# Kernel optimization log

Measured on AMD Instinct MI355X. Metric: run time of the kernel, lower is better.

## Reference

```python
import jax, jax.numpy as jnp
import numpy as np

TOKENS, IN_F, OUT_F = 8192, 4096, 4096

def setup_inputs() -> dict:
    key = jax.random.key(0)
    k1, k2, k3, k4 = jax.random.split(key, 4)
    # int8 activations and weights in [-127, 127]
    x = jax.random.randint(k1, (TOKENS, IN_F), -127, 128, dtype=jnp.int32).astype(jnp.int8)
    weight = jax.random.randint(k2, (OUT_F, IN_F), -127, 128, dtype=jnp.int32).astype(jnp.int8)  # [out, in]
    # static per-output-channel dequant scale (fp16), small so fp16 output doesn't overflow
    dequant_scale = (jax.random.uniform(k3, (OUT_F,), dtype=jnp.float32) * 1e-3).astype(jnp.float16)
    bias = (jax.random.normal(k4, (OUT_F,), dtype=jnp.float32)).astype(jnp.float16)
    return {"x": x, "weight": weight, "dequant_scale": dequant_scale, "bias": bias}

def reference(x, weight, dequant_scale, bias):
    # int8 GEMM with int32 accumulation: [tokens, in] @ [in, out] -> [tokens, out]
    acc = jax.lax.dot_general(
        x, weight.T,
        dimension_numbers=(((1,), (0,)), ((), ())),
        preferred_element_type=jnp.int32,
    )
    # static per-output-channel dequant, cast to fp16, add fp16 bias
    out = (acc.astype(jnp.float32) * dequant_scale.astype(jnp.float32)[None, :]).astype(jnp.float16)
    out = out + bias[None, :]
    # module returns (output, output_bias)
    return (out, bias)
```

## Files before the change

### kernel.cpp

```cpp
#include <hip/hip_runtime.h>
#include <hip/hip_fp16.h>
#include <stdint.h>

typedef __attribute__((ext_vector_type(4))) int int32x4;

#define TOKENS 8192
#define IN_F   4096
#define OUT_F  4096
#define BM 256
#define BN 256
#define BK 128
#define NT (IN_F / BK)

__global__ __launch_bounds__(256)
void pack_kernel(const int* __restrict__ src, uint32_t* __restrict__ dst, int n4)
{
    for (int i = blockIdx.x * 256 + threadIdx.x; i < n4; i += gridDim.x * 256) {
        int32x4 v = ((const int32x4*)src)[i];
        dst[i] = (uint32_t)(v[0] & 0xff) | ((uint32_t)(v[1] & 0xff) << 8) |
                 ((uint32_t)(v[2] & 0xff) << 16) | ((uint32_t)v[3] << 24);
    }
}

__global__ __launch_bounds__(512, 2)
void w8a8_gemm_kernel(const int8_t* __restrict__ x,
                      const int8_t* __restrict__ w,
                      const float* __restrict__ scale,
                      const float* __restrict__ bias,
                      float* __restrict__ out)
{
    __shared__ int8_t lA[2 * 256 * 128];
    __shared__ int8_t lB[2 * 256 * 128];

    const int tid = threadIdx.x;
    const int wv  = tid >> 6;
    const int l   = tid & 63;
    const int wrow = (wv >> 2) * 128;
    const int wcol = (wv & 3) * 64;

    const int bn = blockIdx.x;
    const int bm = blockIdx.y;

    const int8_t* baseA = x + (size_t)bm * BM * IN_F;
    const int8_t* baseB = w + (size_t)bn * BN * IN_F;

    const int seg0 = wv * 2, seg1 = wv * 2 + 1;
    const int r8   = l >> 3;
    const int swc  = (((l & 7) ^ r8) << 4);

    const int fr  = l & 15;
    const int xk  = (l & 7) << 4;
    const int cb0 = (l >> 4) << 4;

    int32x4 acc[8][4];
#pragma unroll
    for (int m = 0; m < 8; ++m)
#pragma unroll
        for (int n = 0; n < 4; ++n)
            acc[m][n] = (int32x4){0, 0, 0, 0};

    int32x4 aF[4][2];
    int32x4 bF[2][2];

    auto stage_half = [&](int h4) {
        const int kt_ = h4 >> 2;
        const int wh_ = h4 & 3;
        const int8_t* sb = (wh_ < 2) ? baseA : baseB;
        int8_t* db = ((wh_ < 2) ? lA : lB) + ((kt_ & 1) << 15) + ((wh_ & 1) << 14);
        const size_t co = (size_t)kt_ * BK + swc;
        const size_t rb = (size_t)((wh_ & 1) * 128 + r8);
        __builtin_amdgcn_global_load_lds(
            (const __attribute__((address_space(1))) void*)(sb + (rb + seg0 * 8) * IN_F + co),
            (__attribute__((address_space(3))) void*)(db + seg0 * 1024), 16, 0, 0);
        __builtin_amdgcn_global_load_lds(
            (const __attribute__((address_space(1))) void*)(sb + (rb + seg1 * 8) * IN_F + co),
            (__attribute__((address_space(3))) void*)(db + seg1 * 1024), 16, 0, 0);
    };
    auto stage_tile = [&](int tt) {
        stage_half(4 * tt + 0); stage_half(4 * tt + 1);
        stage_half(4 * tt + 2); stage_half(4 * tt + 3);
    };

#define LOADA(MH)                                                                     \
    do {                                                                              \
        _Pragma("unroll") for (int j = 0; j < 4; ++j)                                 \
        _Pragma("unroll") for (int ks = 0; ks < 2; ++ks)                              \
            aF[j][ks] = *(const int32x4*)&lAb[(wrow + ((MH)*4 + j) * 16 + fr) * 128 + \
                                              (((ks * 64) + cb0) ^ xk)];              \
    } while (0)

#define LOADB(NH)                                                                     \
    do {                                                                              \
        _Pragma("unroll") for (int j2 = 0; j2 < 2; ++j2)                              \
        _Pragma("unroll") for (int ks = 0; ks < 2; ++ks)                              \
            bF[j2][ks] = *(const int32x4*)&lBb[(wcol + ((NH)*2 + j2) * 16 + fr) * 128 + \
                                               (((ks * 64) + cb0) ^ xk)];             \
    } while (0)

#define MMAQ(MH, NH)                                                                  \
    do {                                                                              \
        _Pragma("unroll") for (int j = 0; j < 4; ++j)                                 \
        _Pragma("unroll") for (int j2 = 0; j2 < 2; ++j2)                              \
        _Pragma("unroll") for (int ks = 0; ks < 2; ++ks)                              \
            acc[(MH)*4 + j][(NH)*2 + j2] = __builtin_amdgcn_mfma_i32_16x16x64_i8(     \
                aF[j][ks], bF[j2][ks], acc[(MH)*4 + j][(NH)*2 + j2], 0, 0, 0);        \
    } while (0)

#define PH(MH, NH)                                                                    \
    do {                                                                              \
        __builtin_amdgcn_s_barrier();                                                 \
        __builtin_amdgcn_s_setprio(1);                                                \
        MMAQ(MH, NH);                                                                 \
        __builtin_amdgcn_s_setprio(0);                                                \
        __builtin_amdgcn_s_barrier();                                                 \
    } while (0)

    stage_tile(0);
    asm volatile("s_waitcnt vmcnt(0)" ::: "memory");
    __builtin_amdgcn_s_barrier();

    for (int t = 0; t < NT; ++t) {
        const int8_t* lAb = lA + ((t & 1) << 15);
        const int8_t* lBb = lB + ((t & 1) << 15);
        const bool pre = (t + 1 < NT);
        if (pre) stage_tile(t + 1);

        LOADA(0); LOADB(0); PH(0, 0);
        LOADB(1);           PH(0, 1);
        LOADA(1);           PH(1, 1);
        LOADB(0);
        __builtin_amdgcn_s_barrier();
        __builtin_amdgcn_s_setprio(1);
        MMAQ(1, 0);
        __builtin_amdgcn_s_setprio(0);
        if (pre) asm volatile("s_waitcnt vmcnt(0)" ::: "memory");
        __builtin_amdgcn_s_barrier();
    }

    const int r0 = (l >> 4) << 2;
#pragma unroll
    for (int n = 0; n < 4; ++n) {
        const int col = bn * BN + wcol + n * 16 + fr;
        const float sc  = scale[col];
        const __half bs = __float2half(bias[col]);
#pragma unroll
        for (int m = 0; m < 8; ++m) {
            const int rowb = bm * BM + wrow + m * 16 + r0;
#pragma unroll
            for (int r = 0; r < 4; ++r) {
                __half h = __float2half((float)acc[m][n][r] * sc);
                out[(size_t)(rowb + r) * OUT_F + col] = __half2float(__hadd(h, bs));
            }
        }
    }
#undef LOADA
#undef LOADB
#undef MMAQ
#undef PH
}

__global__ void bias_copy_kernel(const float* __restrict__ bias, float* __restrict__ dst)
{
    const int i = blockIdx.x * 256 + threadIdx.x;
    if (i < OUT_F) dst[i] = bias[i];
}

extern "C" void kernel_launch(void* const* d_in, const int* in_sizes, int n_in,
                              void* d_out, int out_size, void* d_ws, size_t ws_size,
                              hipStream_t stream)
{
    const int*   x32   = (const int*)d_in[0];
    const int*   w32   = (const int*)d_in[1];
    const float* scale = (const float*)d_in[2];
    const float* bias  = (const float*)d_in[3];
    float* out = (float*)d_out;

    int8_t* x8 = (int8_t*)d_ws;
    int8_t* w8 = x8 + (size_t)TOKENS * IN_F;

    pack_kernel<<<2048, 256, 0, stream>>>(x32, (uint32_t*)x8, TOKENS * IN_F / 4);
    pack_kernel<<<2048, 256, 0, stream>>>(w32, (uint32_t*)w8, OUT_F * IN_F / 4);

    dim3 grid(OUT_F / BN, TOKENS / BM);
    w8a8_gemm_kernel<<<grid, 512, 0, stream>>>(x8, w8, scale, bias, out);
    bias_copy_kernel<<<OUT_F / 256, 256, 0, stream>>>(bias, out + (size_t)TOKENS * OUT_F);
}
```

Baseline: 232.0 us.

## Interleave per-quarter global-to-LDS staging with MFMA phases across two tiles

Reassigns the eight waves to a 4x2 grid, where each wave owns 32x64 sub-blocks in each of the four 128x128 quadrants. The LDS tile loads are split into quarter-tile stages and issued between compute phases, one or two tiles ahead, with partial vmcnt waits instead of a full drain at the end of each iteration. Two B-fragment register sets let one set be reused across phases. The aim is to overlap global loads with MFMA work and avoid the end-of-iteration stall, at the cost of more complex hazard ordering on the double-buffered LDS.

```diff
diff --git a/kernel.cpp b/kernel.cpp
--- a/kernel.cpp
+++ b/kernel.cpp
@@ -29,14 +29,14 @@
                       const float* __restrict__ bias,
                       float* __restrict__ out)
 {
-    __shared__ int8_t lA[2 * 256 * 128];
-    __shared__ int8_t lB[2 * 256 * 128];
+    __shared__ int8_t lA[2 * 2 * 128 * 128];
+    __shared__ int8_t lB[2 * 2 * 128 * 128];
 
     const int tid = threadIdx.x;
     const int wv  = tid >> 6;
     const int l   = tid & 63;
-    const int wrow = (wv >> 2) * 128;
-    const int wcol = (wv & 3) * 64;
+    const int wqm = wv >> 1;
+    const int wqn = wv & 1;
 
     const int bn = blockIdx.x;
     const int bm = blockIdx.y;
@@ -52,15 +52,20 @@
     const int xk  = (l & 7) << 4;
     const int cb0 = (l >> 4) << 4;
 
-    int32x4 acc[8][4];
+    int32x4 acc[2][2][2][4];
 #pragma unroll
-    for (int m = 0; m < 8; ++m)
+    for (int a0 = 0; a0 < 2; ++a0)
 #pragma unroll
-        for (int n = 0; n < 4; ++n)
-            acc[m][n] = (int32x4){0, 0, 0, 0};
+        for (int a1 = 0; a1 < 2; ++a1)
+#pragma unroll
+            for (int a2 = 0; a2 < 2; ++a2)
+#pragma unroll
+                for (int a3 = 0; a3 < 4; ++a3)
+                    acc[a0][a1][a2][a3] = (int32x4){0, 0, 0, 0};
 
-    int32x4 aF[4][2];
-    int32x4 bF[2][2];
+    int32x4 aF[2][2];
+    int32x4 bF0[4][2];
+    int32x4 bF1[4][2];
 
     auto stage_half = [&](int h4) {
         const int kt_ = h4 >> 2;
@@ -76,85 +81,91 @@
             (const __attribute__((address_space(1))) void*)(sb + (rb + seg1 * 8) * IN_F + co),
             (__attribute__((address_space(3))) void*)(db + seg1 * 1024), 16, 0, 0);
     };
-    auto stage_tile = [&](int tt) {
-        stage_half(4 * tt + 0); stage_half(4 * tt + 1);
-        stage_half(4 * tt + 2); stage_half(4 * tt + 3);
-    };
 
-#define LOADA(MH)                                                                     \
-    do {                                                                              \
-        _Pragma("unroll") for (int j = 0; j < 4; ++j)                                 \
-        _Pragma("unroll") for (int ks = 0; ks < 2; ++ks)                              \
-            aF[j][ks] = *(const int32x4*)&lAb[(wrow + ((MH)*4 + j) * 16 + fr) * 128 + \
-                                              (((ks * 64) + cb0) ^ xk)];              \
+#define LDA(MH)                                                                        \
+    do {                                                                               \
+        _Pragma("unroll") for (int mi = 0; mi < 2; ++mi)                               \
+        _Pragma("unroll") for (int ks = 0; ks < 2; ++ks)                               \
+            aF[mi][ks] = *(const int32x4*)&lAb[((MH) << 14) +                          \
+                (wqm * 32 + mi * 16 + fr) * 128 + (((ks * 64) + cb0) ^ xk)];           \
     } while (0)
 
-#define LOADB(NH)                                                                     \
-    do {                                                                              \
-        _Pragma("unroll") for (int j2 = 0; j2 < 2; ++j2)                              \
-        _Pragma("unroll") for (int ks = 0; ks < 2; ++ks)                              \
-            bF[j2][ks] = *(const int32x4*)&lBb[(wcol + ((NH)*2 + j2) * 16 + fr) * 128 + \
-                                               (((ks * 64) + cb0) ^ xk)];             \
+#define LDB(NH, DST)                                                                   \
+    do {                                                                               \
+        _Pragma("unroll") for (int ni = 0; ni < 4; ++ni)                               \
+        _Pragma("unroll") for (int ks = 0; ks < 2; ++ks)                               \
+            DST[ni][ks] = *(const int32x4*)&lBb[((NH) << 14) +                         \
+                (wqn * 64 + ni * 16 + fr) * 128 + (((ks * 64) + cb0) ^ xk)];           \
     } while (0)
 
-#define MMAQ(MH, NH)                                                                  \
-    do {                                                                              \
-        _Pragma("unroll") for (int j = 0; j < 4; ++j)                                 \
-        _Pragma("unroll") for (int j2 = 0; j2 < 2; ++j2)                              \
-        _Pragma("unroll") for (int ks = 0; ks < 2; ++ks)                              \
-            acc[(MH)*4 + j][(NH)*2 + j2] = __builtin_amdgcn_mfma_i32_16x16x64_i8(     \
-                aF[j][ks], bF[j2][ks], acc[(MH)*4 + j][(NH)*2 + j2], 0, 0, 0);        \
+#define MMAQ(MH, NH, BF)                                                               \
+    do {                                                                               \
+        _Pragma("unroll") for (int mi = 0; mi < 2; ++mi)                               \
+        _Pragma("unroll") for (int ni = 0; ni < 4; ++ni)                               \
+        _Pragma("unroll") for (int ks = 0; ks < 2; ++ks)                               \
+            acc[MH][NH][mi][ni] = __builtin_amdgcn_mfma_i32_16x16x64_i8(               \
+                aF[mi][ks], BF[ni][ks], acc[MH][NH][mi][ni], 0, 0, 0);                 \
     } while (0)
 
-#define PH(MH, NH)                                                                    \
-    do {                                                                              \
-        __builtin_amdgcn_s_barrier();                                                 \
-        __builtin_amdgcn_s_setprio(1);                                                \
-        MMAQ(MH, NH);                                                                 \
-        __builtin_amdgcn_s_setprio(0);                                                \
-        __builtin_amdgcn_s_barrier();                                                 \
+#define PH(MH, NH, BF)                                                                 \
+    do {                                                                               \
+        __builtin_amdgcn_s_barrier();                                                  \
+        asm volatile("s_waitcnt lgkmcnt(0)" ::: "memory");                             \
+        __builtin_amdgcn_s_setprio(1);                                                 \
+        MMAQ(MH, NH, BF);                                                              \
+        __builtin_amdgcn_s_setprio(0);                                                 \
+        __builtin_amdgcn_s_barrier();                                                  \
     } while (0)
 
-    stage_tile(0);
-    asm volatile("s_waitcnt vmcnt(0)" ::: "memory");
+    stage_half(0); stage_half(3); stage_half(1); stage_half(2);
+    stage_half(4); stage_half(7);
+    asm volatile("s_waitcnt vmcnt(4)" ::: "memory");
     __builtin_amdgcn_s_barrier();
 
     for (int t = 0; t < NT; ++t) {
         const int8_t* lAb = lA + ((t & 1) << 15);
         const int8_t* lBb = lB + ((t & 1) << 15);
-        const bool pre = (t + 1 < NT);
-        if (pre) stage_tile(t + 1);
 
-        LOADA(0); LOADB(0); PH(0, 0);
-        LOADB(1);           PH(0, 1);
-        LOADA(1);           PH(1, 1);
-        LOADB(0);
-        __builtin_amdgcn_s_barrier();
-        __builtin_amdgcn_s_setprio(1);
-        MMAQ(1, 0);
-        __builtin_amdgcn_s_setprio(0);
-        if (pre) asm volatile("s_waitcnt vmcnt(0)" ::: "memory");
-        __builtin_amdgcn_s_barrier();
+        LDA(0); LDB(0, bF0);
+        if (t + 1 < NT) stage_half(4 * (t + 1) + 1);
+        PH(0, 0, bF0);
+
+        LDB(1, bF1);
+        if (t + 1 < NT) stage_half(4 * (t + 1) + 2);
+        PH(0, 1, bF1);
+
+        LDA(1);
+        if (t + 2 < NT) stage_half(4 * (t + 2) + 0);
+        PH(1, 1, bF1);
+
+        if (t + 2 < NT) stage_half(4 * (t + 2) + 3);
+        if (t + 2 < NT)      asm volatile("s_waitcnt vmcnt(4)" ::: "memory");
+        else if (t + 1 < NT) asm volatile("s_waitcnt vmcnt(0)" ::: "memory");
+        PH(1, 0, bF0);
     }
 
     const int r0 = (l >> 4) << 2;
 #pragma unroll
-    for (int n = 0; n < 4; ++n) {
-        const int col = bn * BN + wcol + n * 16 + fr;
-        const float sc  = scale[col];
-        const __half bs = __float2half(bias[col]);
+    for (int NH = 0; NH < 2; ++NH)
 #pragma unroll
-        for (int m = 0; m < 8; ++m) {
-            const int rowb = bm * BM + wrow + m * 16 + r0;
+        for (int ni = 0; ni < 4; ++ni) {
+            const int col = bn * BN + NH * 128 + wqn * 64 + ni * 16 + fr;
+            const float sc  = scale[col];
+            const __half bs = __float2half(bias[col]);
 #pragma unroll
-            for (int r = 0; r < 4; ++r) {
-                __half h = __float2half((float)acc[m][n][r] * sc);
-                out[(size_t)(rowb + r) * OUT_F + col] = __half2float(__hadd(h, bs));
-            }
+            for (int MH = 0; MH < 2; ++MH)
+#pragma unroll
+                for (int mi = 0; mi < 2; ++mi) {
+                    const int rowb = bm * BM + MH * 128 + wqm * 32 + mi * 16 + r0;
+#pragma unroll
+                    for (int r = 0; r < 4; ++r) {
+                        __half h = __float2half((float)acc[MH][NH][mi][ni][r] * sc);
+                        out[(size_t)(rowb + r) * OUT_F + col] = __half2float(__hadd(h, bs));
+                    }
+                }
         }
-    }
-#undef LOADA
-#undef LOADB
+#undef LDA
+#undef LDB
 #undef MMAQ
 #undef PH
 }
```

After: 211.6 us. 8.8% less time.
